# Optimization experiments

Measured on AMD Instinct MI355X. Metric: run time of the kernel, lower is better.

Reference implementation:

```python
import jax, jax.numpy as jnp
import numpy as np

H = 1024          # hidden_size
I = 2048          # intermediate_size (per routed expert; shared uses I*num_shared)
E = 8             # num_routed_experts
B, S = 2, 1024


def setup_inputs() -> dict:
    key = jax.random.key(0)
    ks = jax.random.split(key, 8)
    sc_h = 1.0 / np.sqrt(H)
    sc_i = 1.0 / np.sqrt(I)
    return {
        "hidden_states": jax.random.normal(ks[0], (B, S, H), jnp.float32),
        "gate_w": jax.random.normal(ks[1], (H, E), jnp.float32) * sc_h,      # router
        "sh_gate": jax.random.normal(ks[2], (H, I), jnp.float32) * sc_h,     # shared SwiGLU
        "sh_up": jax.random.normal(ks[3], (H, I), jnp.float32) * sc_h,
        "sh_down": jax.random.normal(ks[4], (I, H), jnp.float32) * sc_i,
        "rt_gate": jax.random.normal(ks[5], (E, H, I), jnp.float32) * sc_h,  # stacked routed experts
        "rt_up": jax.random.normal(ks[6], (E, H, I), jnp.float32) * sc_h,
        "rt_down": jax.random.normal(ks[7], (E, I, H), jnp.float32) * sc_i,
    }


def _swiglu(x, wg, wu, wd):
    return (jax.nn.silu(x @ wg) * (x @ wu)) @ wd


def reference(hidden_states, gate_w, sh_gate, sh_up, sh_down, rt_gate, rt_up, rt_down):
    b, s, h = hidden_states.shape
    x = hidden_states.reshape(-1, h)                      # [T, H]
    logits = x @ gate_w                                   # [T, E]
    # top-1 routing: score = sigmoid(max logit), expert = argmax
    top_val = jnp.max(logits, axis=-1, keepdims=True)     # [T, 1]
    top_id = jnp.argmax(logits, axis=-1)                  # [T]
    score = jax.nn.sigmoid(top_val)
    xs = x * score                                        # scale tokens BEFORE expert (Llama4)
    # exact dense-masked equivalent of sort/dispatch/per-expert SwiGLU/scatter-combine:
    # every expert is applied to all tokens, then the one-hot mask selects the
    # assigned expert's output per token (identical math to ragged dispatch).
    g = jnp.einsum('th,ehi->eti', xs, rt_gate)            # [E, T, I]
    u = jnp.einsum('th,ehi->eti', xs, rt_up)
    act = jax.nn.silu(g) * u
    y = jnp.einsum('eti,eih->eth', act, rt_down)          # [E, T, H]
    onehot = jax.nn.one_hot(top_id, E, dtype=x.dtype)     # [T, E]
    routed = jnp.einsum('eth,te->th', y, onehot)          # [T, H]
    shared = _swiglu(x, sh_gate, sh_up, sh_down)          # [T, H]
    return (shared + routed).reshape(b, s, h)
```

## Files before the change

kernel.cpp:

```cpp
#include <hip/hip_runtime.h>
#include <cstdint>
#include <cstddef>

#define T_TOK 2048
#define HDIM  1024
#define IDIM  2048
#define NEXP  8

#define BM 128
#define BK1 32
#define BK2 32
#define BN2 64
#define MAXPAD 3072
#define SH_TILES 16
#define RT_TILES 24

typedef __attribute__((ext_vector_type(8))) short short8;
typedef __attribute__((ext_vector_type(4))) short short4v;
typedef __attribute__((ext_vector_type(4))) float float4v;

__device__ __forceinline__ short f2bf(float f) {
  uint32_t u = __float_as_uint(f);
  u += 0x7fffu + ((u >> 16) & 1u);
  return (short)(u >> 16);
}

__device__ __forceinline__ void gload_lds16(const void* g, void* l) {
  __builtin_amdgcn_global_load_lds(
      (const __attribute__((address_space(1))) uint32_t*)g,
      (__attribute__((address_space(3))) uint32_t*)l, 16, 0, 0);
}

__device__ __forceinline__ int swz(int c) { return c ^ ((c >> 4) & 3); }


__global__ __launch_bounds__(256) void zero_init(int* __restrict__ counts,
                                                 int* __restrict__ perm) {
  int i = threadIdx.x;
  if (i < NEXP) counts[i] = 0;
  for (int p = i; p < MAXPAD; p += 256) perm[p] = 0;
}

__global__ __launch_bounds__(256) void router_kernel(
    const float* __restrict__ x, const float* __restrict__ gw,
    short* __restrict__ xbf, short* __restrict__ xsbf,
    int* __restrict__ expert_id, int* __restrict__ slot,
    int* __restrict__ counts) {
  int wv = threadIdx.x >> 6, lane = threadIdx.x & 63;
  int t = blockIdx.x * 4 + wv;
  const float* xr = x + (size_t)t * HDIM;
  float4v xv[4];
  float lg[NEXP];
#pragma unroll
  for (int e = 0; e < NEXP; e++) lg[e] = 0.f;
#pragma unroll
  for (int p = 0; p < 4; p++) {
    xv[p] = *(const float4v*)(xr + p * 256 + lane * 4);
#pragma unroll
    for (int c = 0; c < 4; c++) {
      int h = p * 256 + lane * 4 + c;
      float4v g0 = *(const float4v*)(gw + (size_t)h * NEXP);
      float4v g1 = *(const float4v*)(gw + (size_t)h * NEXP + 4);
      float xc = xv[p][c];
      lg[0] += xc * g0[0]; lg[1] += xc * g0[1];
      lg[2] += xc * g0[2]; lg[3] += xc * g0[3];
      lg[4] += xc * g1[0]; lg[5] += xc * g1[1];
      lg[6] += xc * g1[2]; lg[7] += xc * g1[3];
    }
  }
#pragma unroll
  for (int ofs = 1; ofs < 64; ofs <<= 1) {
#pragma unroll
    for (int e = 0; e < NEXP; e++) lg[e] += __shfl_xor(lg[e], ofs, 64);
  }
  int be = 0;
  float bv = lg[0];
#pragma unroll
  for (int e = 1; e < NEXP; e++) {
    if (lg[e] > bv) { bv = lg[e]; be = e; }
  }
  float score = 1.f / (1.f + __expf(-bv));
  if (lane == 0) {
    expert_id[t] = be;
    slot[t] = atomicAdd(&counts[be], 1);
  }
#pragma unroll
  for (int p = 0; p < 4; p++) {
    short4v b, bs;
#pragma unroll
    for (int c = 0; c < 4; c++) {
      b[c] = f2bf(xv[p][c]);
      bs[c] = f2bf(xv[p][c] * score);
    }
    *(short4v*)(xbf + (size_t)t * HDIM + p * 256 + lane * 4) = b;
    *(short4v*)(xsbf + (size_t)t * HDIM + p * 256 + lane * 4) = bs;
  }
}

__global__ void prefix_kernel(const int* __restrict__ counts, int* __restrict__ pad_off) {
  if (threadIdx.x == 0 && blockIdx.x == 0) {
    int run = 0;
    for (int e = 0; e < NEXP; e++) {
      pad_off[e] = run;
      run += (counts[e] + BM - 1) & ~(BM - 1);
    }
    pad_off[NEXP] = run;
  }
}

__global__ __launch_bounds__(256) void build_perm(
    const int* __restrict__ expert_id, const int* __restrict__ slot,
    const int* __restrict__ pad_off, int* __restrict__ perm) {
  int t = blockIdx.x * 256 + threadIdx.x;
  int e = expert_id[t];
  perm[pad_off[e] + slot[t]] = t;
}


__global__ __launch_bounds__(256) void transpose_all(
    const float* __restrict__ shg, const float* __restrict__ shu,
    const float* __restrict__ rtg, const float* __restrict__ rtu,
    short* __restrict__ shg_t, short* __restrict__ shu_t,
    short* __restrict__ rtg_t, short* __restrict__ rtu_t,
    const float* __restrict__ shd, const float* __restrict__ rtd,
    short* __restrict__ shd_t, short* __restrict__ rtd_t) {
  int bid = blockIdx.x;
  const float* s;
  short* d;
  int R, C, tile_n, tile_r;
  if (bid < 18 * 256) {
    int m = bid >> 8, w = bid & 255;
    R = HDIM; C = IDIM;
    if (m == 0)      { s = shg; d = shg_t; }
    else if (m == 1) { s = shu; d = shu_t; }
    else if (m < 10) { size_t o = (size_t)(m - 2) * HDIM * IDIM; s = rtg + o; d = rtg_t + o; }
    else             { size_t o = (size_t)(m - 10) * HDIM * IDIM; s = rtu + o; d = rtu_t + o; }
    tile_n = w >> 3;
    tile_r = w & 7;
  } else {
    int b2 = bid - 18 * 256;
    int m = b2 >> 8, w = b2 & 255;
    R = IDIM; C = HDIM;
    if (m == 0) { s = shd; d = shd_t; }
    else        { size_t o = (size_t)(m - 1) * IDIM * HDIM; s = rtd + o; d = rtd_t + o; }
    tile_n = w >> 4;
    tile_r = w & 15;
  }
  int lane = threadIdx.x & 63, wv = threadIdx.x >> 6;
  int n0 = tile_n * 64 + (lane & 15) * 4;
  int k0 = tile_r * 128 + wv * 32 + (lane >> 4) * 8;
  float4v v[8];
#pragma unroll
  for (int j = 0; j < 8; j++)
    v[j] = *(const float4v*)(s + (size_t)(k0 + j) * C + n0);
#pragma unroll
  for (int i = 0; i < 4; i++) {
    short8 o;
#pragma unroll
    for (int j = 0; j < 8; j++) o[j] = f2bf(v[j][i]);
    *(short8*)(d + (size_t)(n0 + i) * R + k0) = o;
  }
}


#define G1_STAGE(b, kk) do { \
    gload_lds16(A + gA + (kk), sA[b] + tid * 8);   \
    gload_lds16(Bg + gB + (kk), sBg[b] + tid * 8); \
    gload_lds16(Bu + gB + (kk), sBu[b] + tid * 8); } while (0)

__global__ __launch_bounds__(512, 2) void gemm1_swiglu(
    const short* __restrict__ xbf, const short* __restrict__ xsbf,
    const short* __restrict__ shg_t, const short* __restrict__ shu_t,
    const short* __restrict__ rtg_t, const short* __restrict__ rtu_t,
    short* __restrict__ act_sh, short* __restrict__ act_rt,
    const int* __restrict__ pad_off, const int* __restrict__ perm) {
  __shared__ __align__(1024) short sA[3][BM * BK1];
  __shared__ __align__(1024) short sBg[3][BM * BK1];
  __shared__ __align__(1024) short sBu[3][BM * BK1];
  int tid = threadIdx.x, lane = tid & 63, wv = tid >> 6;
  int C0 = blockIdx.x * 128;
  int y = blockIdx.y;
  const short *A, *Bg, *Bu;
  short* act;
  int R0;
  bool routed = (y >= SH_TILES);
  if (!routed) {
    A = xbf; Bg = shg_t; Bu = shu_t; act = act_sh; R0 = y * BM;
  } else {
    R0 = (y - SH_TILES) * BM;
    if (R0 >= pad_off[NEXP]) return;
    int e = 0;
    while (pad_off[e + 1] <= R0) e++;
    size_t o = (size_t)e * HDIM * IDIM;
    A = xsbf; Bg = rtg_t + o; Bu = rtu_t + o; act = act_rt;
  }
  int c0 = swz(tid);
  int r0c = c0 >> 2;
  int ar0 = routed ? perm[R0 + r0c] : R0 + r0c;
  size_t gA = (size_t)ar0 * HDIM + (c0 & 3) * 8;
  size_t gB = (size_t)(C0 + r0c) * HDIM + (c0 & 3) * 8;

  float4v accg[4][2], accu[4][2];
  float4v z4 = {0.f, 0.f, 0.f, 0.f};
#pragma unroll
  for (int i = 0; i < 4; i++)
#pragma unroll
    for (int j = 0; j < 2; j++) { accg[i][j] = z4; accu[i][j] = z4; }

  const int wrow = (wv >> 2) * 64, wcol = (wv & 3) * 32;
  const int mrow = lane & 15, h4 = lane >> 4;
  int aoff[4], boff[2];
#pragma unroll
  for (int i = 0; i < 4; i++)
    aoff[i] = swz(((wrow + i * 16 + mrow) << 2) + h4) * 8;
#pragma unroll
  for (int j = 0; j < 2; j++)
    boff[j] = swz(((wcol + j * 16 + mrow) << 2) + h4) * 8;

  G1_STAGE(0, 0);
  G1_STAGE(1, BK1);

  int cur = 0;
  for (int k0 = 0; k0 < HDIM; k0 += BK1) {
    if (k0 + BK1 < HDIM) {
      asm volatile("s_waitcnt vmcnt(3)" ::: "memory");
    } else {
      asm volatile("s_waitcnt vmcnt(0)" ::: "memory");
    }
    __builtin_amdgcn_s_barrier();
    int k2 = k0 + 2 * BK1;
    if (k2 < HDIM) {
      int nb = cur + 2; if (nb >= 3) nb -= 3;
      G1_STAGE(nb, k2);
    }
    const short* cA = sA[cur];
    const short* cG = sBg[cur];
    const short* cU = sBu[cur];
    short8 af[4], bg[2], bu[2];
#pragma unroll
    for (int i = 0; i < 4; i++) af[i] = *(const short8*)(cA + aoff[i]);
#pragma unroll
    for (int j = 0; j < 2; j++) {
      bg[j] = *(const short8*)(cG + boff[j]);
      bu[j] = *(const short8*)(cU + boff[j]);
    }
    __builtin_amdgcn_s_setprio(1);
#pragma unroll
    for (int i = 0; i < 4; i++)
#pragma unroll
      for (int j = 0; j < 2; j++) {
        accg[i][j] = __builtin_amdgcn_mfma_f32_16x16x32_bf16(af[i], bg[j], accg[i][j], 0, 0, 0);
        accu[i][j] = __builtin_amdgcn_mfma_f32_16x16x32_bf16(af[i], bu[j], accu[i][j], 0, 0, 0);
      }
    __builtin_amdgcn_s_setprio(0);
    cur = (cur == 2) ? 0 : cur + 1;
  }
  int qrow = h4 * 4, col = mrow;
#pragma unroll
  for (int i = 0; i < 4; i++)
#pragma unroll
    for (int j = 0; j < 2; j++)
#pragma unroll
      for (int r = 0; r < 4; r++) {
        int row = R0 + wrow + i * 16 + qrow + r;
        int c = C0 + wcol + j * 16 + col;
        float g = accg[i][j][r], u = accu[i][j][r];
        float sv = g / (1.f + __expf(-g)) * u;
        act[(size_t)row * IDIM + c] = f2bf(sv);
      }
}


#define G2_STAGE(b, kk) do { \
    gload_lds16(A + gA0 + (kk), sA[b] + tid * 8);         \
    gload_lds16(A + gA1 + (kk), sA[b] + (tid + 256) * 8); \
    gload_lds16(Bd + gB0 + (kk), sB[b] + tid * 8); } while (0)

__global__ __launch_bounds__(256, 4) void gemm2_down(
    const short* __restrict__ act_sh, const short* __restrict__ act_rt,
    const short* __restrict__ shd_t, const short* __restrict__ rtd_t,
    float* __restrict__ out, float* __restrict__ rt_out,
    const int* __restrict__ pad_off, const int* __restrict__ counts,
    const int* __restrict__ perm) {
  __shared__ __align__(1024) short sA[3][BM * BK2];
  __shared__ __align__(1024) short sB[3][BN2 * BK2];
  int tid = threadIdx.x, lane = tid & 63, wv = tid >> 6;
  int C0 = blockIdx.x * BN2;
  int y = blockIdx.y;
  const short *A, *Bd;
  int R0, e = 0;
  bool routed = (y >= SH_TILES);
  if (!routed) {
    A = act_sh; Bd = shd_t; R0 = y * BM;
  } else {
    R0 = (y - SH_TILES) * BM;
    if (R0 >= pad_off[NEXP]) return;
    while (pad_off[e + 1] <= R0) e++;
    A = act_rt; Bd = rtd_t + (size_t)e * IDIM * HDIM;
  }
  int cA0 = swz(tid), cA1 = swz(tid + 256), cB = swz(tid);
  size_t gA0 = (size_t)(R0 + (cA0 >> 2)) * IDIM + (cA0 & 3) * 8;
  size_t gA1 = (size_t)(R0 + (cA1 >> 2)) * IDIM + (cA1 & 3) * 8;
  size_t gB0 = (size_t)(C0 + (cB >> 2)) * IDIM + (cB & 3) * 8;

  float4v acc[2][4];
  float4v z4 = {0.f, 0.f, 0.f, 0.f};
#pragma unroll
  for (int i = 0; i < 2; i++)
#pragma unroll
    for (int j = 0; j < 4; j++) acc[i][j] = z4;

  const int wrow = wv * 32;
  const int mrow = lane & 15, h4 = lane >> 4;
  int aoff[2], boff[4];
#pragma unroll
  for (int i = 0; i < 2; i++)
    aoff[i] = swz(((wrow + i * 16 + mrow) << 2) + h4) * 8;
#pragma unroll
  for (int j = 0; j < 4; j++)
    boff[j] = swz(((j * 16 + mrow) << 2) + h4) * 8;

  G2_STAGE(0, 0);
  G2_STAGE(1, BK2);

  int cur = 0;
  for (int k0 = 0; k0 < IDIM; k0 += BK2) {
    if (k0 + BK2 < IDIM) {
      asm volatile("s_waitcnt vmcnt(3)" ::: "memory");
    } else {
      asm volatile("s_waitcnt vmcnt(0)" ::: "memory");
    }
    __builtin_amdgcn_s_barrier();
    int k2 = k0 + 2 * BK2;
    if (k2 < IDIM) {
      int nb = cur + 2; if (nb >= 3) nb -= 3;
      G2_STAGE(nb, k2);
    }
    const short* cAp = sA[cur];
    const short* cBp = sB[cur];
    short8 af[2], bf4[4];
#pragma unroll
    for (int i = 0; i < 2; i++) af[i] = *(const short8*)(cAp + aoff[i]);
#pragma unroll
    for (int j = 0; j < 4; j++) bf4[j] = *(const short8*)(cBp + boff[j]);
    __builtin_amdgcn_s_setprio(1);
#pragma unroll
    for (int i = 0; i < 2; i++)
#pragma unroll
      for (int j = 0; j < 4; j++)
        acc[i][j] = __builtin_amdgcn_mfma_f32_16x16x32_bf16(af[i], bf4[j], acc[i][j], 0, 0, 0);
    __builtin_amdgcn_s_setprio(0);
    cur = (cur == 2) ? 0 : cur + 1;
  }
  int qrow = h4 * 4, col = mrow;
#pragma unroll
  for (int i = 0; i < 2; i++)
#pragma unroll
    for (int j = 0; j < 4; j++)
#pragma unroll
      for (int r = 0; r < 4; r++) {
        int row = R0 + wrow + i * 16 + qrow + r;
        int c = C0 + j * 16 + col;
        float v = acc[i][j][r];
        if (!routed) {
          out[(size_t)row * HDIM + c] = v;
        } else if (row - pad_off[e] < counts[e]) {
          rt_out[(size_t)perm[row] * HDIM + c] = v;
        }
      }
}

__global__ __launch_bounds__(256) void add_routed(float* __restrict__ out,
                                                  const float* __restrict__ rt_out) {
  size_t i = ((size_t)blockIdx.x * 256 + threadIdx.x) * 4;
  float4v a = *(const float4v*)(out + i);
  float4v b = *(const float4v*)(rt_out + i);
  a[0] += b[0]; a[1] += b[1]; a[2] += b[2]; a[3] += b[3];
  *(float4v*)(out + i) = a;
}


extern "C" void kernel_launch(void* const* d_in, const int* in_sizes, int n_in,
                              void* d_out, int out_size, void* d_ws, size_t ws_size,
                              hipStream_t stream) {
  const float* x       = (const float*)d_in[0];
  const float* gate_w  = (const float*)d_in[1];
  const float* sh_gate = (const float*)d_in[2];
  const float* sh_up   = (const float*)d_in[3];
  const float* sh_down = (const float*)d_in[4];
  const float* rt_gate = (const float*)d_in[5];
  const float* rt_up   = (const float*)d_in[6];
  const float* rt_down = (const float*)d_in[7];
  float* out = (float*)d_out;

  char* w = (char*)d_ws;
  const size_t MB = 1024 * 1024;
  short* xbf    = (short*)(w + 0 * MB);
  short* xsbf   = (short*)(w + 4 * MB);
  short* act_sh = (short*)(w + 8 * MB);
  short* act_rt = (short*)(w + 16 * MB);
  float* rt_out = (float*)(w + 28 * MB);
  short* shg_t  = (short*)(w + 36 * MB);
  short* shu_t  = (short*)(w + 40 * MB);
  short* shd_t  = (short*)(w + 44 * MB);
  short* rtg_t  = (short*)(w + 48 * MB);
  short* rtu_t  = (short*)(w + 80 * MB);
  short* rtd_t  = (short*)(w + 112 * MB);
  int* ints     = (int*)(w + 144 * MB);
  int* counts    = ints;
  int* pad_off   = ints + 8;
  int* expert_id = ints + 32;
  int* slot      = ints + 32 + 2048;
  int* perm      = ints + 32 + 4096;

  zero_init<<<1, 256, 0, stream>>>(counts, perm);
  router_kernel<<<T_TOK / 4, 256, 0, stream>>>(x, gate_w, xbf, xsbf, expert_id, slot, counts);
  prefix_kernel<<<1, 64, 0, stream>>>(counts, pad_off);
  build_perm<<<T_TOK / 256, 256, 0, stream>>>(expert_id, slot, pad_off, perm);

  transpose_all<<<18 * 256 + 9 * 256, 256, 0, stream>>>(
      sh_gate, sh_up, rt_gate, rt_up, shg_t, shu_t, rtg_t, rtu_t,
      sh_down, rt_down, shd_t, rtd_t);

  gemm1_swiglu<<<dim3(IDIM / 128, SH_TILES + RT_TILES), 512, 0, stream>>>(
      xbf, xsbf, shg_t, shu_t, rtg_t, rtu_t, act_sh, act_rt, pad_off, perm);

  gemm2_down<<<dim3(HDIM / BN2, SH_TILES + RT_TILES), 256, 0, stream>>>(
      act_sh, act_rt, shd_t, rtd_t, out, rt_out, pad_off, counts, perm);

  add_routed<<<(T_TOK * HDIM) / (256 * 4), 256, 0, stream>>>(out, rt_out);
}
```

Baseline: 413.3 us.

## Pre-tile transposed bf16 weights so GEMM B-tile loads are contiguous

```diff
diff --git a/kernel.cpp b/kernel.cpp
--- a/kernel.cpp
+++ b/kernel.cpp
@@ -124,49 +124,75 @@
     short* __restrict__ rtg_t, short* __restrict__ rtu_t,
     const float* __restrict__ shd, const float* __restrict__ rtd,
     short* __restrict__ shd_t, short* __restrict__ rtd_t) {
-  int bid = blockIdx.x;
-  const float* s;
-  short* d;
-  int R, C, tile_n, tile_r;
+  __shared__ short tl[8704];
+  int bid = blockIdx.x, t = threadIdx.x;
   if (bid < 18 * 256) {
     int m = bid >> 8, w = bid & 255;
-    R = HDIM; C = IDIM;
+    const float* s; short* d;
     if (m == 0)      { s = shg; d = shg_t; }
     else if (m == 1) { s = shu; d = shu_t; }
     else if (m < 10) { size_t o = (size_t)(m - 2) * HDIM * IDIM; s = rtg + o; d = rtg_t + o; }
     else             { size_t o = (size_t)(m - 10) * HDIM * IDIM; s = rtu + o; d = rtu_t + o; }
-    tile_n = w >> 3;
-    tile_r = w & 7;
+    int nt = w >> 4, ktp = w & 15;
+    int n0 = nt * 128, k0 = ktp * 64;
+#pragma unroll
+    for (int j = 0; j < 8; j++) {
+      int flat = j * 256 + t;
+      int row = flat >> 5, c16 = flat & 31;
+      float4v v = *(const float4v*)(s + (size_t)(k0 + row) * IDIM + n0 + c16 * 4);
+      short4v b;
+#pragma unroll
+      for (int c = 0; c < 4; c++) b[c] = f2bf(v[c]);
+      *(short4v*)(&tl[row * 132 + c16 * 4]) = b;
+    }
+    __syncthreads();
+#pragma unroll
+    for (int j = 0; j < 4; j++) {
+      int c2 = j * 256 + t;
+      int kt2 = c2 >> 9, c = c2 & 511;
+      int n = c >> 2, kg = c & 3;
+      short8 o;
+#pragma unroll
+      for (int i = 0; i < 8; i++) o[i] = tl[(kt2 * 32 + kg * 8 + i) * 132 + n];
+      *(short8*)(d + (size_t)(nt * 32 + ktp * 2 + kt2) * 4096 + (size_t)c * 8) = o;
+    }
   } else {
     int b2 = bid - 18 * 256;
     int m = b2 >> 8, w = b2 & 255;
-    R = IDIM; C = HDIM;
+    const float* s; short* d;
     if (m == 0) { s = shd; d = shd_t; }
     else        { size_t o = (size_t)(m - 1) * IDIM * HDIM; s = rtd + o; d = rtd_t + o; }
-    tile_n = w >> 4;
-    tile_r = w & 15;
-  }
-  int lane = threadIdx.x & 63, wv = threadIdx.x >> 6;
-  int n0 = tile_n * 64 + (lane & 15) * 4;
-  int k0 = tile_r * 128 + wv * 32 + (lane >> 4) * 8;
-  float4v v[8];
-#pragma unroll
-  for (int j = 0; j < 8; j++)
-    v[j] = *(const float4v*)(s + (size_t)(k0 + j) * C + n0);
-#pragma unroll
-  for (int i = 0; i < 4; i++) {
-    short8 o;
-#pragma unroll
-    for (int j = 0; j < 8; j++) o[j] = f2bf(v[j][i]);
-    *(short8*)(d + (size_t)(n0 + i) * R + k0) = o;
+    int nt = w >> 4, ktq = w & 15;
+    int n0 = nt * 64, k0 = ktq * 128;
+#pragma unroll
+    for (int j = 0; j < 8; j++) {
+      int flat = j * 256 + t;
+      int row = flat >> 4, c16 = flat & 15;
+      float4v v = *(const float4v*)(s + (size_t)(k0 + row) * HDIM + n0 + c16 * 4);
+      short4v b;
+#pragma unroll
+      for (int c = 0; c < 4; c++) b[c] = f2bf(v[c]);
+      *(short4v*)(&tl[row * 68 + c16 * 4]) = b;
+    }
+    __syncthreads();
+#pragma unroll
+    for (int j = 0; j < 4; j++) {
+      int c2 = j * 256 + t;
+      int kq2 = c2 >> 8, c = c2 & 255;
+      int n = c >> 2, kg = c & 3;
+      short8 o;
+#pragma unroll
+      for (int i = 0; i < 8; i++) o[i] = tl[(kq2 * 32 + kg * 8 + i) * 68 + n];
+      *(short8*)(d + (size_t)(nt * 64 + ktq * 4 + kq2) * 2048 + (size_t)c * 8) = o;
+    }
   }
 }
 
 
 #define G1_STAGE(b, kk) do { \
-    gload_lds16(A + gA + (kk), sA[b] + tid * 8);   \
-    gload_lds16(Bg + gB + (kk), sBg[b] + tid * 8); \
-    gload_lds16(Bu + gB + (kk), sBu[b] + tid * 8); } while (0)
+    gload_lds16(A + gA + (kk), sA[b] + tid * 8);                    \
+    gload_lds16(Bg + gB + (size_t)(kk) * 128, sBg[b] + tid * 8);    \
+    gload_lds16(Bu + gB + (size_t)(kk) * 128, sBu[b] + tid * 8); } while (0)
 
 __global__ __launch_bounds__(512, 2) void gemm1_swiglu(
     const short* __restrict__ xbf, const short* __restrict__ xsbf,
@@ -178,7 +204,6 @@
   __shared__ __align__(1024) short sBg[3][BM * BK1];
   __shared__ __align__(1024) short sBu[3][BM * BK1];
   int tid = threadIdx.x, lane = tid & 63, wv = tid >> 6;
-  int C0 = blockIdx.x * 128;
   int y = blockIdx.y;
   const short *A, *Bg, *Bu;
   short* act;
@@ -194,11 +219,12 @@
     size_t o = (size_t)e * HDIM * IDIM;
     A = xsbf; Bg = rtg_t + o; Bu = rtu_t + o; act = act_rt;
   }
+  int C0 = blockIdx.x * 128;
   int c0 = swz(tid);
   int r0c = c0 >> 2;
   int ar0 = routed ? perm[R0 + r0c] : R0 + r0c;
   size_t gA = (size_t)ar0 * HDIM + (c0 & 3) * 8;
-  size_t gB = (size_t)(C0 + r0c) * HDIM + (c0 & 3) * 8;
+  size_t gB = (size_t)blockIdx.x * 32 * 4096 + (size_t)c0 * 8;
 
   float4v accg[4][2], accu[4][2];
   float4v z4 = {0.f, 0.f, 0.f, 0.f};
@@ -274,7 +300,7 @@
 #define G2_STAGE(b, kk) do { \
     gload_lds16(A + gA0 + (kk), sA[b] + tid * 8);         \
     gload_lds16(A + gA1 + (kk), sA[b] + (tid + 256) * 8); \
-    gload_lds16(Bd + gB0 + (kk), sB[b] + tid * 8); } while (0)
+    gload_lds16(Bd + gB0 + (size_t)(kk) * 64, sB[b] + tid * 8); } while (0)
 
 __global__ __launch_bounds__(256, 4) void gemm2_down(
     const short* __restrict__ act_sh, const short* __restrict__ act_rt,
@@ -301,7 +327,7 @@
   int cA0 = swz(tid), cA1 = swz(tid + 256), cB = swz(tid);
   size_t gA0 = (size_t)(R0 + (cA0 >> 2)) * IDIM + (cA0 & 3) * 8;
   size_t gA1 = (size_t)(R0 + (cA1 >> 2)) * IDIM + (cA1 & 3) * 8;
-  size_t gB0 = (size_t)(C0 + (cB >> 2)) * IDIM + (cB & 3) * 8;
+  size_t gB0 = (size_t)blockIdx.x * 64 * 2048 + (size_t)cB * 8;
 
   float4v acc[2][4];
   float4v z4 = {0.f, 0.f, 0.f, 0.f};
```

New measurement: 406.8 us. No clear change (-1.6%).
